# Kernel optimization log

Hardware: AMD Instinct MI355X
Metric: run time of the kernel (lower is better)

Reference implementation:

```python
import jax, jax.numpy as jnp
import numpy as np

NUM_EMBEDDINGS = 1024
EMBEDDING_DIM = 256
COMMITMENT_COST = 1.0


def setup_inputs() -> dict:
    key = jax.random.key(0)
    k_in, k_emb = jax.random.split(key)
    inputs = jax.random.normal(k_in, (64, 32, 32, EMBEDDING_DIM), dtype=jnp.float32)
    embeddings = jax.random.normal(k_emb, (NUM_EMBEDDINGS, EMBEDDING_DIM), dtype=jnp.float32)
    return {"inputs": inputs, "embeddings": embeddings}


def reference(inputs, embeddings):
    # Eval-mode forward of VectorQuantizerEMA (EMA buffer update is a no-grad
    # stateful side effect, skipped here; see notes).
    input_shape = inputs.shape
    flat = inputs.reshape(-1, EMBEDDING_DIM)                       # [N, D]
    distances = (
        jnp.sum(flat ** 2, axis=1, keepdims=True)
        + jnp.sum(embeddings ** 2, axis=1)
        - 2.0 * flat @ embeddings.T
    )
    encoding_indices = jnp.argmin(distances, axis=1)               # [N]
    # one-hot @ embeddings == gather (avoid materializing [N, K] one-hot)
    quantized = embeddings[encoding_indices].reshape(input_shape)
    e_latent_loss = jnp.mean((jax.lax.stop_gradient(quantized) - inputs) ** 2)
    loss = COMMITMENT_COST * e_latent_loss
    # straight-through estimator
    quantized_st = inputs + jax.lax.stop_gradient(quantized - inputs)
    return quantized_st, loss, encoding_indices[:, None]
```

## Files before the change

### kernel.cpp

```cpp
#include <hip/hip_runtime.h>
#include <float.h>

#define NROWS 65536
#define DK 256
#define NCODES 1024
#define FLAG_CAP 8192
#define MARGIN1 0.15f
#define D_BIAS 384.0f

#define LOSS_OFF 16777216
#define IDX_OFF  16777217

#define CHUNK_STRIDE 1040

#define WS_FLAG1   0
#define WS_LOSSP   8
#define WS_ENORMD  520
#define WS_ENORMF  8712
#define WS_FROWS   12808
#define WS_IDX     45576
#define WS_EHI     307728

typedef _Float16 f16x8 __attribute__((ext_vector_type(8)));
typedef float f32x4 __attribute__((ext_vector_type(4)));
typedef unsigned int uint32;

__device__ __forceinline__ uint32 packh2(float a, float b) {
  return (uint32)__builtin_bit_cast(unsigned short, (_Float16)a) |
         ((uint32)__builtin_bit_cast(unsigned short, (_Float16)b) << 16);
}

__global__ __launch_bounds__(256) void init_kernel(
    const float* __restrict__ E, double* __restrict__ enorm_d,
    float* __restrict__ enorm_f, uint4* __restrict__ Ehi,
    int* __restrict__ flag1, double* __restrict__ loss_part) {
  const int t = threadIdx.x;
  const int c = blockIdx.x * 8 + (t >> 5);
  const int g = t & 31;
  if (blockIdx.x == 0) {
    if (t == 0) *flag1 = 0;
    if (t < 64) loss_part[t] = 0.0;
  }
  const float4* er4 = (const float4*)(E + (size_t)c * DK);
  const float4 va = er4[g * 2];
  const float4 vb = er4[g * 2 + 1];
  double s = (double)va.x * va.x + (double)va.y * va.y + (double)va.z * va.z + (double)va.w * va.w
           + (double)vb.x * vb.x + (double)vb.y * vb.y + (double)vb.z * vb.z + (double)vb.w * vb.w;
  uint4 h;
  h.x = packh2(va.x, va.y);
  h.y = packh2(va.z, va.w);
  h.z = packh2(vb.x, vb.y);
  h.w = packh2(vb.z, vb.w);
  const int ctg = c >> 8, cga = (c >> 4) & 15, col = c & 15;
  const int kc = g >> 2, quad = g & 3;
  Ehi[((size_t)((ctg * 8 + kc) * 16 + cga)) * 64 + (size_t)(quad * 16 + col)] = h;
  #pragma unroll
  for (int m = 1; m < 32; m <<= 1) s += __shfl_xor(s, m, 64);
  if (g == 0) {
    enorm_d[c] = s;
    enorm_f[c] = (float)s;
  }
}

__global__ __launch_bounds__(256, 4) void dist_fused(
    const float* __restrict__ X, const uint4* __restrict__ Ehi,
    const float* __restrict__ E, const float* __restrict__ enorm_f,
    int* __restrict__ idx_ws, int* __restrict__ flag1, int* __restrict__ flag_rows,
    float* __restrict__ out, double* __restrict__ loss_part) {
  __shared__ __attribute__((aligned(16))) char lds[33280];
  const int tid = threadIdx.x;
  const int lane = tid & 63;
  const int wid = tid >> 6;
  const int col = lane & 15;
  const int rowBase = blockIdx.x * 64;

  {
    const float4* X4 = (const float4*)X + (size_t)rowBase * 64;
    #pragma unroll
    for (int i = 0; i < 16; ++i) {
      const int f4 = i * 256 + tid;
      const int row = f4 >> 6;
      const int k0 = (f4 & 63) << 2;
      const float4 v = X4[f4];
      uint2 p;
      p.x = packh2(v.x, v.y);
      p.y = packh2(v.z, v.w);
      const int chunk = (row >> 4) * 8 + (k0 >> 5);
      const int off = chunk * CHUNK_STRIDE
                      + (((k0 >> 3) & 3) * 16 + (row & 15)) * 16
                      + ((k0 >> 2) & 1) * 8;
      *(uint2*)(lds + off) = p;
    }
  }
  __syncthreads();

  float rv1[16], rv2[16];
  #pragma unroll
  for (int i = 0; i < 16; ++i) { rv1[i] = FLT_MAX; rv2[i] = FLT_MAX; }

  for (int ctg = 0; ctg < 4; ++ctg) {
    f32x4 acc[4][4];
    #pragma unroll
    for (int rg = 0; rg < 4; ++rg)
      #pragma unroll
      for (int cg = 0; cg < 4; ++cg) acc[rg][cg] = (f32x4){0.f, 0.f, 0.f, 0.f};

    #pragma unroll 2
    for (int ks = 0; ks < 8; ++ks) {
      const size_t ub = ((size_t)((ctg * 8 + ks) * 16 + wid * 4)) * 64 + (size_t)lane;
      f16x8 a[4], bh[4];
      #pragma unroll
      for (int cg = 0; cg < 4; ++cg) bh[cg] = *(const f16x8*)&Ehi[ub + (size_t)cg * 64];
      #pragma unroll
      for (int rg = 0; rg < 4; ++rg)
        a[rg] = *(const f16x8*)(lds + (rg * 8 + ks) * CHUNK_STRIDE + lane * 16);
      #pragma unroll
      for (int rg = 0; rg < 4; ++rg)
        #pragma unroll
        for (int cg = 0; cg < 4; ++cg)
          acc[rg][cg] = __builtin_amdgcn_mfma_f32_16x16x32_f16(a[rg], bh[cg], acc[rg][cg], 0, 0, 0);
    }
    #pragma unroll
    for (int cg = 0; cg < 4; ++cg) {
      const int code = ctg * 256 + wid * 64 + cg * 16 + col;
      const float en = enorm_f[code] + D_BIAS;
      const uint32 li = (uint32)((ctg << 6) | (cg << 4) | col);
      #pragma unroll
      for (int rg = 0; rg < 4; ++rg)
        #pragma unroll
        for (int reg = 0; reg < 4; ++reg) {
          const int i = rg * 4 + reg;
          const float d = fmaf(-2.0f, acc[rg][cg][reg], en);
          const float p = __builtin_bit_cast(float,
              (__builtin_bit_cast(uint32, d) & 0xFFFFFF00u) | li);
          rv2[i] = fminf(rv2[i], fmaxf(rv1[i], p));
          rv1[i] = fminf(rv1[i], p);
        }
    }
  }

  #pragma unroll
  for (int i = 0; i < 16; ++i) {
    #pragma unroll
    for (int m = 1; m < 16; m <<= 1) {
      const float o1 = __shfl_xor(rv1[i], m, 64);
      const float o2 = __shfl_xor(rv2[i], m, 64);
      rv2[i] = fminf(fminf(rv2[i], o2), fmaxf(rv1[i], o1));
      rv1[i] = fminf(rv1[i], o1);
    }
  }

  __syncthreads();
  float* M = (float*)lds;
  int* idxs = (int*)(lds + 4096);
  if (col == 0) {
    const int quad = lane >> 4;
    #pragma unroll
    for (int i = 0; i < 16; ++i) {
      const int row = (i >> 2) * 16 + quad * 4 + (i & 3);
      M[(row * 4 + wid) * 2 + 0] = rv1[i];
      M[(row * 4 + wid) * 2 + 1] = rv2[i];
    }
  }
  __syncthreads();
  if (tid < 64) {
    const float a1 = M[(tid * 4 + 0) * 2], a2 = M[(tid * 4 + 0) * 2 + 1];
    const float b1 = M[(tid * 4 + 1) * 2], b2 = M[(tid * 4 + 1) * 2 + 1];
    const float c1 = M[(tid * 4 + 2) * 2], c2 = M[(tid * 4 + 2) * 2 + 1];
    const float d1 = M[(tid * 4 + 3) * 2], d2 = M[(tid * 4 + 3) * 2 + 1];
    const float lo1 = fminf(a1, b1), hi1 = fmaxf(a1, b1);
    const float lo2 = fminf(c1, d1), hi2 = fmaxf(c1, d1);
    const float r1 = fminf(lo1, lo2);
    const float s1 = fminf(fmaxf(lo1, lo2), fminf(hi1, hi2));
    const float r2 = fminf(fminf(fminf(a2, b2), fminf(c2, d2)), s1);
    const int w1 = (r1 == a1) ? 0 : (r1 == b1) ? 1 : (r1 == c1) ? 2 : 3;
    const uint32 u1 = __builtin_bit_cast(uint32, r1);
    const int li = (int)(u1 & 255u);
    const int code = ((li >> 6) & 3) * 256 + w1 * 64 + ((li >> 4) & 3) * 16 + (li & 15);
    const int row = rowBase + tid;
    idxs[tid] = code;
    idx_ws[row] = code;
    out[IDX_OFF + row] = (float)code;
    const float q1 = __builtin_bit_cast(float, u1 & 0xFFFFFF00u);
    const float q2 = __builtin_bit_cast(float, __builtin_bit_cast(uint32, r2) & 0xFFFFFF00u);
    if (q2 - q1 < MARGIN1) {
      const int p = atomicAdd(flag1, 1);
      if (p < FLAG_CAP) flag_rows[p] = row;
    }
  }
  __syncthreads();

  const int rsub = tid >> 6, c4 = tid & 63;
  double ls = 0.0;
  #pragma unroll 4
  for (int i = 0; i < 16; ++i) {
    const int rl = i * 4 + rsub;
    const int row = rowBase + rl;
    const int idx = idxs[rl];
    const float4 q = ((const float4*)E)[(size_t)idx * 64 + c4];
    const float4 x = ((const float4*)X)[(size_t)row * 64 + c4];
    ((float4*)out)[(size_t)row * 64 + c4] = q;
    const double d0 = (double)q.x - (double)x.x;
    const double d1 = (double)q.y - (double)x.y;
    const double d2 = (double)q.z - (double)x.z;
    const double d3 = (double)q.w - (double)x.w;
    ls += d0 * d0 + d1 * d1 + d2 * d2 + d3 * d3;
  }
  #pragma unroll
  for (int o = 32; o > 0; o >>= 1) ls += __shfl_down(ls, o, 64);
  __shared__ double wsum[4];
  if ((tid & 63) == 0) wsum[tid >> 6] = ls;
  __syncthreads();
  if (tid == 0)
    atomicAdd(&loss_part[blockIdx.x & 63], wsum[0] + wsum[1] + wsum[2] + wsum[3]);
}

__global__ __launch_bounds__(256) void fixup64(
    const float* __restrict__ X, const float* __restrict__ E,
    const double* __restrict__ enorm_d, const int* __restrict__ flag1,
    const int* __restrict__ flag_rows, const int* __restrict__ idx_ws,
    float* __restrict__ out, double* __restrict__ loss_part) {
  __shared__ float xs[4][256];
  __shared__ double rv[256];
  __shared__ int ri[256];
  __shared__ int rowsh[4], oldsh[4], newsh[4];
  __shared__ double dold_sh[4], dnew_sh[4];
  int cnt = *flag1;
  if (cnt > FLAG_CAP) cnt = FLAG_CAP;
  const int fbase = blockIdx.x * 4;
  if (fbase >= cnt) return;
  const int nr = min(4, cnt - fbase);
  if (threadIdx.x < 4) {
    const int r = threadIdx.x;
    const int row = (r < nr) ? flag_rows[fbase + r] : flag_rows[fbase];
    rowsh[r] = row;
    oldsh[r] = idx_ws[row];
  }
  __syncthreads();
  for (int e = threadIdx.x; e < 4 * 256; e += 256) {
    const int r = e >> 8, k = e & 255;
    xs[r][k] = X[(size_t)rowsh[r] * DK + k];
  }
  __syncthreads();
  double best[4] = {1e300, 1e300, 1e300, 1e300};
  int bi[4] = {0x7fffffff, 0x7fffffff, 0x7fffffff, 0x7fffffff};
  for (int cc = 0; cc < 4; ++cc) {
    const int c = cc * 256 + threadIdx.x;
    const float4* E4 = (const float4*)(E + (size_t)c * DK);
    double s0 = 0.0, s1 = 0.0, s2 = 0.0, s3 = 0.0;
    #pragma unroll 4
    for (int q = 0; q < 64; ++q) {
      const float4 ev = E4[q];
      const float4 x0 = ((const float4*)xs[0])[q];
      const float4 x1 = ((const float4*)xs[1])[q];
      const float4 x2 = ((const float4*)xs[2])[q];
      const float4 x3 = ((const float4*)xs[3])[q];
      s0 += (double)ev.x * x0.x + (double)ev.y * x0.y + (double)ev.z * x0.z + (double)ev.w * x0.w;
      s1 += (double)ev.x * x1.x + (double)ev.y * x1.y + (double)ev.z * x1.z + (double)ev.w * x1.w;
      s2 += (double)ev.x * x2.x + (double)ev.y * x2.y + (double)ev.z * x2.z + (double)ev.w * x2.w;
      s3 += (double)ev.x * x3.x + (double)ev.y * x3.y + (double)ev.z * x3.z + (double)ev.w * x3.w;
    }
    const double en = enorm_d[c];
    const double dd[4] = {en - 2.0 * s0, en - 2.0 * s1, en - 2.0 * s2, en - 2.0 * s3};
    #pragma unroll
    for (int r = 0; r < 4; ++r) {
      if (dd[r] < best[r]) { best[r] = dd[r]; bi[r] = c; }
      if (c == oldsh[r]) dold_sh[r] = dd[r];
    }
  }
  for (int r = 0; r < nr; ++r) {
    rv[threadIdx.x] = best[r];
    ri[threadIdx.x] = bi[r];
    __syncthreads();
    for (int off = 128; off > 0; off >>= 1) {
      if (threadIdx.x < off) {
        const double ov = rv[threadIdx.x + off];
        const int oi = ri[threadIdx.x + off];
        if (ov < rv[threadIdx.x] || (ov == rv[threadIdx.x] && oi < ri[threadIdx.x])) {
          rv[threadIdx.x] = ov;
          ri[threadIdx.x] = oi;
        }
      }
      __syncthreads();
    }
    if (threadIdx.x == 0) { dnew_sh[r] = rv[0]; newsh[r] = ri[0]; }
    __syncthreads();
  }
  for (int r = 0; r < nr; ++r) {
    const int newi = newsh[r];
    if (newi != oldsh[r]) {
      const int row = rowsh[r];
      out[(size_t)row * DK + threadIdx.x] = E[(size_t)newi * DK + threadIdx.x];
      if (threadIdx.x == 0) {
        out[IDX_OFF + row] = (float)newi;
        atomicAdd(&loss_part[row & 63], dnew_sh[r] - dold_sh[r]);
      }
    }
  }
}

__global__ __launch_bounds__(64) void finalize(
    const double* __restrict__ loss_part, float* __restrict__ out) {
  double v = loss_part[threadIdx.x];
  for (int o = 32; o > 0; o >>= 1) v += __shfl_down(v, o, 64);
  if (threadIdx.x == 0) out[LOSS_OFF] = (float)(v / 16777216.0);
}

extern "C" void kernel_launch(void* const* d_in, const int* in_sizes, int n_in,
                              void* d_out, int out_size, void* d_ws, size_t ws_size,
                              hipStream_t stream) {
  const float* X = (const float*)d_in[0];
  const float* E = (const float*)d_in[1];
  float* out = (float*)d_out;
  char* ws = (char*)d_ws;

  int*    flag1     = (int*)(ws + WS_FLAG1);
  double* loss_part = (double*)(ws + WS_LOSSP);
  double* enorm_d   = (double*)(ws + WS_ENORMD);
  float*  enorm_f   = (float*)(ws + WS_ENORMF);
  int*    flag_rows = (int*)(ws + WS_FROWS);
  int*    idx_ws    = (int*)(ws + WS_IDX);
  uint4*  Ehi       = (uint4*)(ws + WS_EHI);

  hipLaunchKernelGGL(init_kernel, dim3(128), dim3(256), 0, stream,
                     E, enorm_d, enorm_f, Ehi, flag1, loss_part);
  hipLaunchKernelGGL(dist_fused, dim3(NROWS / 64), dim3(256), 0, stream,
                     X, Ehi, E, enorm_f, idx_ws, flag1, flag_rows, out, loss_part);
  hipLaunchKernelGGL(fixup64, dim3(FLAG_CAP / 4), dim3(256), 0, stream,
                     X, E, enorm_d, flag1, flag_rows, idx_ws, out, loss_part);
  hipLaunchKernelGGL(finalize, dim3(1), dim3(64), 0, stream, loss_part, out);
}
```

Before: 228.4 us.

## Rescore flagged rows in fp32 with LDS-tiled codebook, fallback to fp64 on near-ties

The fixup kernel now computes distances for flagged rows in fp32, staging codebook tiles in LDS with an XOR swizzle instead of doing a full fp64 dot product over all codes. It tracks the best and second-best distance per row and reruns the old fp64 scan only when the gap is below a small tie threshold. The loss correction is now computed directly from element differences instead of from the fp64 distance values. The aim is to cut fp64 arithmetic cost. The risk is a wrong argmin if the fp32 gap is misjudged, and the extra LDS use lowers occupancy.

```diff
diff --git a/kernel.cpp b/kernel.cpp
--- a/kernel.cpp
+++ b/kernel.cpp
@@ -7,6 +7,7 @@
 #define FLAG_CAP 8192
 #define MARGIN1 0.15f
 #define D_BIAS 384.0f
+#define TIE_EPS 2.0e-3f
 
 #define LOSS_OFF 16777216
 #define IDX_OFF  16777217
@@ -217,84 +218,183 @@
 
 __global__ __launch_bounds__(256) void fixup64(
     const float* __restrict__ X, const float* __restrict__ E,
-    const double* __restrict__ enorm_d, const int* __restrict__ flag1,
-    const int* __restrict__ flag_rows, const int* __restrict__ idx_ws,
-    float* __restrict__ out, double* __restrict__ loss_part) {
-  __shared__ float xs[4][256];
+    const double* __restrict__ enorm_d, const float* __restrict__ enorm_f,
+    const int* __restrict__ flag1, const int* __restrict__ flag_rows,
+    const int* __restrict__ idx_ws, float* __restrict__ out,
+    double* __restrict__ loss_part) {
+  __shared__ __attribute__((aligned(16))) float xs[4][256];
+  __shared__ float4 es[2048];
   __shared__ double rv[256];
   __shared__ int ri[256];
+  __shared__ float wv1[4][4], wv2[4][4];
+  __shared__ int wi1[4][4];
+  __shared__ float fin1[4], fin2[4];
+  __shared__ int fini[4];
   __shared__ int rowsh[4], oldsh[4], newsh[4];
-  __shared__ double dold_sh[4], dnew_sh[4];
+
   int cnt = *flag1;
   if (cnt > FLAG_CAP) cnt = FLAG_CAP;
   const int fbase = blockIdx.x * 4;
   if (fbase >= cnt) return;
   const int nr = min(4, cnt - fbase);
-  if (threadIdx.x < 4) {
-    const int r = threadIdx.x;
-    const int row = (r < nr) ? flag_rows[fbase + r] : flag_rows[fbase];
-    rowsh[r] = row;
-    oldsh[r] = idx_ws[row];
-  }
-  __syncthreads();
-  for (int e = threadIdx.x; e < 4 * 256; e += 256) {
-    const int r = e >> 8, k = e & 255;
-    xs[r][k] = X[(size_t)rowsh[r] * DK + k];
-  }
-  __syncthreads();
-  double best[4] = {1e300, 1e300, 1e300, 1e300};
-  int bi[4] = {0x7fffffff, 0x7fffffff, 0x7fffffff, 0x7fffffff};
+  const int tid = threadIdx.x;
+  if (tid < 4) {
+    const int row = (tid < nr) ? flag_rows[fbase + tid] : flag_rows[fbase];
+    rowsh[tid] = row;
+    oldsh[tid] = idx_ws[row];
+  }
+  __syncthreads();
+  for (int e = tid; e < 4 * 256; e += 256)
+    xs[e >> 8][e & 255] = X[(size_t)rowsh[e >> 8] * DK + (e & 255)];
+  __syncthreads();
+
+  const float4* E4g = (const float4*)E;
+  float acc[4][4];
+  #pragma unroll
+  for (int cc = 0; cc < 4; ++cc)
+    #pragma unroll
+    for (int r = 0; r < 4; ++r) acc[cc][r] = 0.f;
+
+  const int f_st = tid & 7;
+  const int rr_st = tid >> 3;
+  const int sw = tid & 7;
+
+  for (int kb = 0; kb < 8; ++kb) {
+    float4 xr[4][8];
+    #pragma unroll
+    for (int r = 0; r < 4; ++r)
+      #pragma unroll
+      for (int f = 0; f < 8; ++f)
+        xr[r][f] = ((const float4*)xs[r])[kb * 8 + f];
+    #pragma unroll
+    for (int cc = 0; cc < 4; ++cc) {
+      __syncthreads();
+      #pragma unroll
+      for (int p = 0; p < 8; ++p) {
+        const int r = p * 32 + rr_st;
+        es[r * 8 + (f_st ^ (r & 7))] = E4g[(size_t)(cc * 256 + r) * 64 + kb * 8 + f_st];
+      }
+      __syncthreads();
+      #pragma unroll
+      for (int f = 0; f < 8; ++f) {
+        const float4 e4 = es[tid * 8 + (f ^ sw)];
+        #pragma unroll
+        for (int r = 0; r < 4; ++r)
+          acc[cc][r] += e4.x * xr[r][f].x + e4.y * xr[r][f].y
+                      + e4.z * xr[r][f].z + e4.w * xr[r][f].w;
+      }
+    }
+  }
+
+  float v1[4], v2[4];
+  int i1[4];
+  #pragma unroll
+  for (int r = 0; r < 4; ++r) { v1[r] = FLT_MAX; v2[r] = FLT_MAX; i1[r] = 0; }
+  #pragma unroll
   for (int cc = 0; cc < 4; ++cc) {
-    const int c = cc * 256 + threadIdx.x;
-    const float4* E4 = (const float4*)(E + (size_t)c * DK);
-    double s0 = 0.0, s1 = 0.0, s2 = 0.0, s3 = 0.0;
-    #pragma unroll 4
-    for (int q = 0; q < 64; ++q) {
-      const float4 ev = E4[q];
-      const float4 x0 = ((const float4*)xs[0])[q];
-      const float4 x1 = ((const float4*)xs[1])[q];
-      const float4 x2 = ((const float4*)xs[2])[q];
-      const float4 x3 = ((const float4*)xs[3])[q];
-      s0 += (double)ev.x * x0.x + (double)ev.y * x0.y + (double)ev.z * x0.z + (double)ev.w * x0.w;
-      s1 += (double)ev.x * x1.x + (double)ev.y * x1.y + (double)ev.z * x1.z + (double)ev.w * x1.w;
-      s2 += (double)ev.x * x2.x + (double)ev.y * x2.y + (double)ev.z * x2.z + (double)ev.w * x2.w;
-      s3 += (double)ev.x * x3.x + (double)ev.y * x3.y + (double)ev.z * x3.z + (double)ev.w * x3.w;
-    }
-    const double en = enorm_d[c];
-    const double dd[4] = {en - 2.0 * s0, en - 2.0 * s1, en - 2.0 * s2, en - 2.0 * s3};
+    const int code = cc * 256 + tid;
+    const float en = enorm_f[code];
     #pragma unroll
     for (int r = 0; r < 4; ++r) {
-      if (dd[r] < best[r]) { best[r] = dd[r]; bi[r] = c; }
-      if (c == oldsh[r]) dold_sh[r] = dd[r];
-    }
-  }
+      const float d = fmaf(-2.0f, acc[cc][r], en);
+      if (d < v1[r]) { v2[r] = v1[r]; v1[r] = d; i1[r] = code; }
+      else v2[r] = fminf(v2[r], d);
+    }
+  }
+
+  const int lane = tid & 63, wid = tid >> 6;
+  #pragma unroll
+  for (int r = 0; r < 4; ++r) {
+    float b1 = v1[r], b2 = v2[r];
+    int bi = i1[r];
+    #pragma unroll
+    for (int m = 1; m < 64; m <<= 1) {
+      const float o1 = __shfl_xor(b1, m, 64);
+      const float o2 = __shfl_xor(b2, m, 64);
+      const int oi = __shfl_xor(bi, m, 64);
+      const float hi = fmaxf(b1, o1);
+      b2 = fminf(fminf(b2, o2), hi);
+      if (o1 < b1 || (o1 == b1 && oi < bi)) { b1 = o1; bi = oi; }
+    }
+    if (lane == 0) { wv1[wid][r] = b1; wi1[wid][r] = bi; wv2[wid][r] = b2; }
+  }
+  __syncthreads();
+  if (tid < 4) {
+    float b1 = wv1[0][tid], b2 = wv2[0][tid];
+    int bi = wi1[0][tid];
+    #pragma unroll
+    for (int w = 1; w < 4; ++w) {
+      const float o1 = wv1[w][tid], o2 = wv2[w][tid];
+      const int oi = wi1[w][tid];
+      b2 = fminf(fminf(b2, o2), fmaxf(b1, o1));
+      if (o1 < b1 || (o1 == b1 && oi < bi)) { b1 = o1; bi = oi; }
+    }
+    fin1[tid] = b1;
+    fin2[tid] = b2;
+    fini[tid] = bi;
+    newsh[tid] = bi;
+  }
+  __syncthreads();
+
   for (int r = 0; r < nr; ++r) {
-    rv[threadIdx.x] = best[r];
-    ri[threadIdx.x] = bi[r];
-    __syncthreads();
-    for (int off = 128; off > 0; off >>= 1) {
-      if (threadIdx.x < off) {
-        const double ov = rv[threadIdx.x + off];
-        const int oi = ri[threadIdx.x + off];
-        if (ov < rv[threadIdx.x] || (ov == rv[threadIdx.x] && oi < ri[threadIdx.x])) {
-          rv[threadIdx.x] = ov;
-          ri[threadIdx.x] = oi;
+    if (fin2[r] - fin1[r] < TIE_EPS) {
+      double bd = 1e300;
+      int bi_ = 0x7fffffff;
+      for (int cc = 0; cc < 4; ++cc) {
+        const int c = cc * 256 + tid;
+        const float4* Er = (const float4*)(E + (size_t)c * DK);
+        double s = 0.0;
+        #pragma unroll 4
+        for (int q = 0; q < 64; ++q) {
+          const float4 ev = Er[q];
+          const float4 xv = ((const float4*)xs[r])[q];
+          s += (double)ev.x * xv.x + (double)ev.y * xv.y
+             + (double)ev.z * xv.z + (double)ev.w * xv.w;
         }
-      }
-      __syncthreads();
-    }
-    if (threadIdx.x == 0) { dnew_sh[r] = rv[0]; newsh[r] = ri[0]; }
-    __syncthreads();
-  }
+        const double dd = enorm_d[c] - 2.0 * s;
+        if (dd < bd) { bd = dd; bi_ = c; }
+      }
+      rv[tid] = bd;
+      ri[tid] = bi_;
+      __syncthreads();
+      for (int off = 128; off > 0; off >>= 1) {
+        if (tid < off) {
+          const double ov = rv[tid + off];
+          const int oi = ri[tid + off];
+          if (ov < rv[tid] || (ov == rv[tid] && oi < ri[tid])) {
+            rv[tid] = ov;
+            ri[tid] = oi;
+          }
+        }
+        __syncthreads();
+      }
+      if (tid == 0) newsh[r] = ri[0];
+      __syncthreads();
+    }
+  }
+
   for (int r = 0; r < nr; ++r) {
     const int newi = newsh[r];
-    if (newi != oldsh[r]) {
+    const int oldi = oldsh[r];
+    if (newi != oldi) {
       const int row = rowsh[r];
-      out[(size_t)row * DK + threadIdx.x] = E[(size_t)newi * DK + threadIdx.x];
-      if (threadIdx.x == 0) {
+      const float ev = E[(size_t)newi * DK + tid];
+      const float eo = E[(size_t)oldi * DK + tid];
+      const float x = xs[r][tid];
+      out[(size_t)row * DK + tid] = ev;
+      const double dn = (double)ev - (double)x;
+      const double dl = (double)eo - (double)x;
+      rv[tid] = dn * dn - dl * dl;
+      __syncthreads();
+      for (int off = 128; off > 0; off >>= 1) {
+        if (tid < off) rv[tid] += rv[tid + off];
+        __syncthreads();
+      }
+      if (tid == 0) {
         out[IDX_OFF + row] = (float)newi;
-        atomicAdd(&loss_part[row & 63], dnew_sh[r] - dold_sh[r]);
-      }
+        atomicAdd(&loss_part[row & 63], rv[0]);
+      }
+      __syncthreads();
     }
   }
 }
@@ -327,6 +427,6 @@
   hipLaunchKernelGGL(dist_fused, dim3(NROWS / 64), dim3(256), 0, stream,
                      X, Ehi, E, enorm_f, idx_ws, flag1, flag_rows, out, loss_part);
   hipLaunchKernelGGL(fixup64, dim3(FLAG_CAP / 4), dim3(256), 0, stream,
-                     X, E, enorm_d, flag1, flag_rows, idx_ws, out, loss_part);
+                     X, E, enorm_d, enorm_f, flag1, flag_rows, idx_ws, out, loss_part);
   hipLaunchKernelGGL(finalize, dim3(1), dim3(64), 0, stream, loss_part, out);
 }
```

Result: slower. 291.5 us (+27.6%).

## Double-buffer codebook loads in distance GEMM and rewrite fixup with fp32 screening

Applied to the files above, without the earlier changes.

The main MFMA loop is flattened into 32 k-steps with codebook fragments prefetched one step ahead (ping-pong registers), and the two-smallest tracking now uses fmed3. The minimum occupancy hint drops from 4 to 3 waves to leave room for the extra registers. The fixup kernel becomes one row per 1024-thread block reading a transposed fp32 codebook built by a new transpose kernel. It screens candidates in fp32 and only falls back to a fp64 re-evaluation when the top two distances fall within a tie epsilon; the loss delta is recomputed directly. A risk is that Et is placed at the same workspace offset as Ehi, so the transpose overwrites Ehi after dist_fused has finished with it.

```diff
diff --git a/kernel.cpp b/kernel.cpp
--- a/kernel.cpp
+++ b/kernel.cpp
@@ -7,6 +7,7 @@
 #define FLAG_CAP 8192
 #define MARGIN1 0.15f
 #define D_BIAS 384.0f
+#define TIE_EPS 2.0e-3f
 
 #define LOSS_OFF 16777216
 #define IDX_OFF  16777217
@@ -16,10 +17,11 @@
 #define WS_FLAG1   0
 #define WS_LOSSP   8
 #define WS_ENORMD  520
-#define WS_ENORMF  8712
-#define WS_FROWS   12808
-#define WS_IDX     45576
+#define WS_ENORMF  8720
+#define WS_FROWS   12816
+#define WS_IDX     45584
 #define WS_EHI     307728
+#define WS_ET      307728
 
 typedef _Float16 f16x8 __attribute__((ext_vector_type(8)));
 typedef float f32x4 __attribute__((ext_vector_type(4)));
@@ -62,7 +64,7 @@
   }
 }
 
-__global__ __launch_bounds__(256, 4) void dist_fused(
+__global__ __launch_bounds__(256, 3) void dist_fused(
     const float* __restrict__ X, const uint4* __restrict__ Ehi,
     const float* __restrict__ E, const float* __restrict__ enorm_f,
     int* __restrict__ idx_ws, int* __restrict__ flag1, int* __restrict__ flag_rows,
@@ -98,28 +100,32 @@
   #pragma unroll
   for (int i = 0; i < 16; ++i) { rv1[i] = FLT_MAX; rv2[i] = FLT_MAX; }
 
-  for (int ctg = 0; ctg < 4; ++ctg) {
-    f32x4 acc[4][4];
+  f32x4 acc[4][4];
+  #pragma unroll
+  for (int rg = 0; rg < 4; ++rg)
+    #pragma unroll
+    for (int cg = 0; cg < 4; ++cg) acc[rg][cg] = (f32x4){0.f, 0.f, 0.f, 0.f};
+
+  f16x8 bhA[4], bhB[4];
+  auto loadB_ = [&](int t, f16x8* bh) {
+    const size_t ub = ((size_t)(t * 16 + wid * 4)) * 64 + (size_t)lane;
+    #pragma unroll
+    for (int cg = 0; cg < 4; ++cg) bh[cg] = *(const f16x8*)&Ehi[ub + (size_t)cg * 64];
+  };
+  auto loadA_ = [&](int t, f16x8* av) {
+    const int ks = t & 7;
+    #pragma unroll
+    for (int rg = 0; rg < 4; ++rg)
+      av[rg] = *(const f16x8*)(lds + (rg * 8 + ks) * CHUNK_STRIDE + lane * 16);
+  };
+  auto domfma = [&](f16x8* av, f16x8* bh) {
     #pragma unroll
     for (int rg = 0; rg < 4; ++rg)
       #pragma unroll
-      for (int cg = 0; cg < 4; ++cg) acc[rg][cg] = (f32x4){0.f, 0.f, 0.f, 0.f};
-
-    #pragma unroll 2
-    for (int ks = 0; ks < 8; ++ks) {
-      const size_t ub = ((size_t)((ctg * 8 + ks) * 16 + wid * 4)) * 64 + (size_t)lane;
-      f16x8 a[4], bh[4];
-      #pragma unroll
-      for (int cg = 0; cg < 4; ++cg) bh[cg] = *(const f16x8*)&Ehi[ub + (size_t)cg * 64];
-      #pragma unroll
-      for (int rg = 0; rg < 4; ++rg)
-        a[rg] = *(const f16x8*)(lds + (rg * 8 + ks) * CHUNK_STRIDE + lane * 16);
-      #pragma unroll
-      for (int rg = 0; rg < 4; ++rg)
-        #pragma unroll
-        for (int cg = 0; cg < 4; ++cg)
-          acc[rg][cg] = __builtin_amdgcn_mfma_f32_16x16x32_f16(a[rg], bh[cg], acc[rg][cg], 0, 0, 0);
-    }
+      for (int cg = 0; cg < 4; ++cg)
+        acc[rg][cg] = __builtin_amdgcn_mfma_f32_16x16x32_f16(av[rg], bh[cg], acc[rg][cg], 0, 0, 0);
+  };
+  auto epilogue = [&](int ctg) {
     #pragma unroll
     for (int cg = 0; cg < 4; ++cg) {
       const int code = ctg * 256 + wid * 64 + cg * 16 + col;
@@ -130,13 +136,29 @@
         #pragma unroll
         for (int reg = 0; reg < 4; ++reg) {
           const int i = rg * 4 + reg;
-          const float d = fmaf(-2.0f, acc[rg][cg][reg], en);
+          const float dd = fmaf(-2.0f, acc[rg][cg][reg], en);
           const float p = __builtin_bit_cast(float,
-              (__builtin_bit_cast(uint32, d) & 0xFFFFFF00u) | li);
-          rv2[i] = fminf(rv2[i], fmaxf(rv1[i], p));
+              (__builtin_bit_cast(uint32, dd) & 0xFFFFFF00u) | li);
+          rv2[i] = __builtin_amdgcn_fmed3f(p, rv1[i], rv2[i]);
           rv1[i] = fminf(rv1[i], p);
         }
     }
+    #pragma unroll
+    for (int rg = 0; rg < 4; ++rg)
+      #pragma unroll
+      for (int cg = 0; cg < 4; ++cg) acc[rg][cg] = (f32x4){0.f, 0.f, 0.f, 0.f};
+  };
+
+  loadB_(0, bhA);
+  f16x8 av[4];
+  for (int tt = 0; tt < 32; tt += 2) {
+    loadB_(tt + 1, bhB);
+    loadA_(tt, av);
+    domfma(av, bhA);
+    if (tt + 2 < 32) loadB_(tt + 2, bhA);
+    loadA_(tt + 1, av);
+    domfma(av, bhB);
+    if (((tt + 1) & 7) == 7) epilogue(tt >> 3);
   }
 
   #pragma unroll
@@ -215,87 +237,148 @@
     atomicAdd(&loss_part[blockIdx.x & 63], wsum[0] + wsum[1] + wsum[2] + wsum[3]);
 }
 
-__global__ __launch_bounds__(256) void fixup64(
+__global__ __launch_bounds__(256) void transposeE(
+    const float* __restrict__ E, float* __restrict__ Et) {
+  __shared__ float tile[64][65];
+  const int t = threadIdx.x;
+  const int c0 = (blockIdx.x & 15) * 64;
+  const int k0 = (blockIdx.x >> 4) * 64;
+  {
+    const int c = t & 63, q = t >> 6;
+    const float4* src = (const float4*)(E + (size_t)(c0 + c) * DK + k0 + q * 16);
+    #pragma unroll
+    for (int j = 0; j < 4; ++j) {
+      const float4 v = src[j];
+      const int kk = q * 16 + j * 4;
+      tile[kk + 0][c] = v.x;
+      tile[kk + 1][c] = v.y;
+      tile[kk + 2][c] = v.z;
+      tile[kk + 3][c] = v.w;
+    }
+  }
+  __syncthreads();
+  {
+    const int kk = t >> 2, cq = (t & 3) * 16;
+    float4* dst = (float4*)(Et + (size_t)(k0 + kk) * NCODES + c0 + cq);
+    #pragma unroll
+    for (int j = 0; j < 4; ++j) {
+      dst[j] = (float4){tile[kk][cq + j * 4 + 0], tile[kk][cq + j * 4 + 1],
+                        tile[kk][cq + j * 4 + 2], tile[kk][cq + j * 4 + 3]};
+    }
+  }
+}
+
+__global__ __launch_bounds__(1024) void fixup_row(
     const float* __restrict__ X, const float* __restrict__ E,
-    const double* __restrict__ enorm_d, const int* __restrict__ flag1,
+    const float* __restrict__ Et, const double* __restrict__ enorm_d,
+    const float* __restrict__ enorm_f, const int* __restrict__ flag1,
     const int* __restrict__ flag_rows, const int* __restrict__ idx_ws,
     float* __restrict__ out, double* __restrict__ loss_part) {
-  __shared__ float xs[4][256];
-  __shared__ double rv[256];
-  __shared__ int ri[256];
-  __shared__ int rowsh[4], oldsh[4], newsh[4];
-  __shared__ double dold_sh[4], dnew_sh[4];
+  __shared__ float xk_s[256];
+  __shared__ float w1s[16], w2s[16];
+  __shared__ int wis[16];
+  __shared__ double dvs[16];
+  __shared__ int dis[16];
+  __shared__ double red[256];
+  __shared__ int new_sh;
+  __shared__ float g1s, g2s;
+  const int tid = threadIdx.x;
+  const int lane = tid & 63, wid = tid >> 6;
   int cnt = *flag1;
   if (cnt > FLAG_CAP) cnt = FLAG_CAP;
-  const int fbase = blockIdx.x * 4;
-  if (fbase >= cnt) return;
-  const int nr = min(4, cnt - fbase);
-  if (threadIdx.x < 4) {
-    const int r = threadIdx.x;
-    const int row = (r < nr) ? flag_rows[fbase + r] : flag_rows[fbase];
-    rowsh[r] = row;
-    oldsh[r] = idx_ws[row];
-  }
-  __syncthreads();
-  for (int e = threadIdx.x; e < 4 * 256; e += 256) {
-    const int r = e >> 8, k = e & 255;
-    xs[r][k] = X[(size_t)rowsh[r] * DK + k];
-  }
-  __syncthreads();
-  double best[4] = {1e300, 1e300, 1e300, 1e300};
-  int bi[4] = {0x7fffffff, 0x7fffffff, 0x7fffffff, 0x7fffffff};
-  for (int cc = 0; cc < 4; ++cc) {
-    const int c = cc * 256 + threadIdx.x;
-    const float4* E4 = (const float4*)(E + (size_t)c * DK);
-    double s0 = 0.0, s1 = 0.0, s2 = 0.0, s3 = 0.0;
+  for (int r = blockIdx.x; r < cnt; r += gridDim.x) {
+    const int row = flag_rows[r];
+    const int oldi = idx_ws[row];
+    __syncthreads();
+    if (tid < 256) xk_s[tid] = X[(size_t)row * DK + tid];
+    __syncthreads();
+
+    const float* Ecol = Et + tid;
+    float a0 = 0.f, a1 = 0.f, a2 = 0.f, a3 = 0.f;
     #pragma unroll 4
-    for (int q = 0; q < 64; ++q) {
-      const float4 ev = E4[q];
-      const float4 x0 = ((const float4*)xs[0])[q];
-      const float4 x1 = ((const float4*)xs[1])[q];
-      const float4 x2 = ((const float4*)xs[2])[q];
-      const float4 x3 = ((const float4*)xs[3])[q];
-      s0 += (double)ev.x * x0.x + (double)ev.y * x0.y + (double)ev.z * x0.z + (double)ev.w * x0.w;
-      s1 += (double)ev.x * x1.x + (double)ev.y * x1.y + (double)ev.z * x1.z + (double)ev.w * x1.w;
-      s2 += (double)ev.x * x2.x + (double)ev.y * x2.y + (double)ev.z * x2.z + (double)ev.w * x2.w;
-      s3 += (double)ev.x * x3.x + (double)ev.y * x3.y + (double)ev.z * x3.z + (double)ev.w * x3.w;
-    }
-    const double en = enorm_d[c];
-    const double dd[4] = {en - 2.0 * s0, en - 2.0 * s1, en - 2.0 * s2, en - 2.0 * s3};
-    #pragma unroll
-    for (int r = 0; r < 4; ++r) {
-      if (dd[r] < best[r]) { best[r] = dd[r]; bi[r] = c; }
-      if (c == oldsh[r]) dold_sh[r] = dd[r];
-    }
-  }
-  for (int r = 0; r < nr; ++r) {
-    rv[threadIdx.x] = best[r];
-    ri[threadIdx.x] = bi[r];
+    for (int k = 0; k < 256; k += 4) {
+      a0 = fmaf(Ecol[(size_t)k * NCODES], xk_s[k], a0);
+      a1 = fmaf(Ecol[(size_t)(k + 1) * NCODES], xk_s[k + 1], a1);
+      a2 = fmaf(Ecol[(size_t)(k + 2) * NCODES], xk_s[k + 2], a2);
+      a3 = fmaf(Ecol[(size_t)(k + 3) * NCODES], xk_s[k + 3], a3);
+    }
+    const float d = fmaf(-2.0f, (a0 + a1) + (a2 + a3), enorm_f[tid]);
+
+    float b1 = d, b2 = FLT_MAX;
+    int i1_ = tid;
+    #pragma unroll
+    for (int m = 1; m < 64; m <<= 1) {
+      const float o1 = __shfl_xor(b1, m, 64);
+      const float o2 = __shfl_xor(b2, m, 64);
+      const int oi = __shfl_xor(i1_, m, 64);
+      b2 = fminf(fminf(b2, o2), fmaxf(b1, o1));
+      if (o1 < b1 || (o1 == b1 && oi < i1_)) { b1 = o1; i1_ = oi; }
+    }
+    if (lane == 0) { w1s[wid] = b1; w2s[wid] = b2; wis[wid] = i1_; }
     __syncthreads();
-    for (int off = 128; off > 0; off >>= 1) {
-      if (threadIdx.x < off) {
-        const double ov = rv[threadIdx.x + off];
-        const int oi = ri[threadIdx.x + off];
-        if (ov < rv[threadIdx.x] || (ov == rv[threadIdx.x] && oi < ri[threadIdx.x])) {
-          rv[threadIdx.x] = ov;
-          ri[threadIdx.x] = oi;
-        }
-      }
+    if (tid == 0) {
+      float B1 = w1s[0], B2 = w2s[0];
+      int I1 = wis[0];
+      #pragma unroll
+      for (int w = 1; w < 16; ++w) {
+        B2 = fminf(fminf(B2, w2s[w]), fmaxf(B1, w1s[w]));
+        if (w1s[w] < B1 || (w1s[w] == B1 && wis[w] < I1)) { B1 = w1s[w]; I1 = wis[w]; }
+      }
+      new_sh = I1;
+      g1s = B1;
+      g2s = B2;
+    }
+    __syncthreads();
+    int newi = new_sh;
+
+    if (g2s - g1s < TIE_EPS) {
+      double s = 0.0;
+      #pragma unroll 8
+      for (int k = 0; k < 256; ++k)
+        s += (double)Ecol[(size_t)k * NCODES] * (double)xk_s[k];
+      double bd = enorm_d[tid] - 2.0 * s;
+      int bi_ = tid;
+      #pragma unroll
+      for (int m = 1; m < 64; m <<= 1) {
+        const double ov = __shfl_xor(bd, m, 64);
+        const int oi = __shfl_xor(bi_, m, 64);
+        if (ov < bd || (ov == bd && oi < bi_)) { bd = ov; bi_ = oi; }
+      }
+      if (lane == 0) { dvs[wid] = bd; dis[wid] = bi_; }
       __syncthreads();
-    }
-    if (threadIdx.x == 0) { dnew_sh[r] = rv[0]; newsh[r] = ri[0]; }
+      if (tid == 0) {
+        double B = dvs[0];
+        int I = dis[0];
+        #pragma unroll
+        for (int w = 1; w < 16; ++w)
+          if (dvs[w] < B || (dvs[w] == B && dis[w] < I)) { B = dvs[w]; I = dis[w]; }
+        new_sh = I;
+      }
+      __syncthreads();
+      newi = new_sh;
+    }
+
+    if (newi != oldi) {
+      if (tid < 256) {
+        const float x = xk_s[tid];
+        const float ev = E[(size_t)newi * DK + tid];
+        const float eo = E[(size_t)oldi * DK + tid];
+        out[(size_t)row * DK + tid] = ev;
+        const double dn = (double)ev - (double)x;
+        const double dl = (double)eo - (double)x;
+        red[tid] = dn * dn - dl * dl;
+      }
+      __syncthreads();
+      for (int off = 128; off > 0; off >>= 1) {
+        if (tid < off) red[tid] += red[tid + off];
+        __syncthreads();
+      }
+      if (tid == 0) {
+        out[IDX_OFF + row] = (float)newi;
+        atomicAdd(&loss_part[row & 63], red[0]);
+      }
+    }
     __syncthreads();
-  }
-  for (int r = 0; r < nr; ++r) {
-    const int newi = newsh[r];
-    if (newi != oldsh[r]) {
-      const int row = rowsh[r];
-      out[(size_t)row * DK + threadIdx.x] = E[(size_t)newi * DK + threadIdx.x];
-      if (threadIdx.x == 0) {
-        out[IDX_OFF + row] = (float)newi;
-        atomicAdd(&loss_part[row & 63], dnew_sh[r] - dold_sh[r]);
-      }
-    }
   }
 }
 
@@ -321,12 +404,15 @@
   int*    flag_rows = (int*)(ws + WS_FROWS);
   int*    idx_ws    = (int*)(ws + WS_IDX);
   uint4*  Ehi       = (uint4*)(ws + WS_EHI);
+  float*  Et        = (float*)(ws + WS_ET);
 
   hipLaunchKernelGGL(init_kernel, dim3(128), dim3(256), 0, stream,
                      E, enorm_d, enorm_f, Ehi, flag1, loss_part);
   hipLaunchKernelGGL(dist_fused, dim3(NROWS / 64), dim3(256), 0, stream,
                      X, Ehi, E, enorm_f, idx_ws, flag1, flag_rows, out, loss_part);
-  hipLaunchKernelGGL(fixup64, dim3(FLAG_CAP / 4), dim3(256), 0, stream,
-                     X, E, enorm_d, flag1, flag_rows, idx_ws, out, loss_part);
+  hipLaunchKernelGGL(transposeE, dim3(64), dim3(256), 0, stream, E, Et);
+  hipLaunchKernelGGL(fixup_row, dim3(1024), dim3(1024), 0, stream,
+                     X, E, Et, enorm_d, enorm_f, flag1, flag_rows, idx_ws,
+                     out, loss_part);
   hipLaunchKernelGGL(finalize, dim3(1), dim3(64), 0, stream, loss_part, out);
 }
```

After: 236.2 us. +3.4%, slower.
